# Performance work log

Measured on AMD Instinct MI355X. Metric: run time of the kernel, lower is better.

The kernel has to match this reference:

```python
import jax, jax.numpy as jnp
import numpy as np

B, H, S, D = 2, 16, 2048, 64
SCALE = 1.0 / (D ** 0.5)
MASK_FILL = -1e9


def setup_inputs() -> dict:
    key = jax.random.key(0)
    kq, kk, kv = jax.random.split(key, 3)
    q = jax.random.normal(kq, (B, H, S, D), dtype=jnp.float32)
    k = jax.random.normal(kk, (B, H, S, D), dtype=jnp.float32)
    v = jax.random.normal(kv, (B, H, S, D), dtype=jnp.float32)
    # causal mask: True where attention is disallowed (j > i)
    attn_mask = jnp.triu(jnp.ones((S, S), dtype=jnp.bool_), k=1)[None, None]
    return {"q": q, "k": k, "v": v, "attn_mask": attn_mask}


def reference(q, k, v, attn_mask):
    # scores: [B,H,S,S] = (q @ k^T) * scale, then masked_fill(mask, -1e9)
    scores = jnp.einsum("bhqd,bhkd->bhqk", q, k) * SCALE
    scores = jnp.where(attn_mask, MASK_FILL, scores)
    attn_prob = jax.nn.softmax(scores, axis=-1)  # dropout p=0.0 (eval)
    context = jnp.einsum("bhqk,bhkd->bhqd", attn_prob, v)
    return (context, attn_prob)
```

## Files before the change

### kernel.cpp

```cpp
#include <hip/hip_runtime.h>

#define NB 2
#define NH 16
#define SS 2048
#define DD 64
constexpr float kScale = 0.125f;

typedef __attribute__((ext_vector_type(8))) short bf16x8;
typedef __attribute__((ext_vector_type(4))) float f32x4;

union FragAB { bf16x8 v; unsigned u[4]; };

__device__ __forceinline__ unsigned pack2bf(float lo, float hi) {
  unsigned ul = __float_as_uint(lo) + 0x8000u;
  unsigned uh = __float_as_uint(hi) + 0x8000u;
  return __builtin_amdgcn_perm(uh, ul, 0x07060302u);
}
__device__ __forceinline__ short f2bf(float f) {
  return (short)((__float_as_uint(f) + 0x8000u) >> 16);
}

__global__ __launch_bounds__(256, 3) void attn_mfma(
    const float* __restrict__ Q, const float* __restrict__ K,
    const float* __restrict__ V, float* __restrict__ ctx,
    float* __restrict__ prob) {
  const int qt   = 31 - (blockIdx.x & 31);
  const int bh   = blockIdx.x >> 5;
  const int t    = threadIdx.x;
  const int lane = t & 63;
  const int wave = t >> 6;
  const int quad = lane >> 4;
  const int l16  = lane & 15;

  const int q_base = qt * 64;
  const int i_max  = q_base + 63;
  const int qw     = q_base + wave * 16;
  const size_t hoff = (size_t)bh * SS * DD;
  const float* Kh = K + hoff;
  const float* Vh = V + hoff;

  __shared__ __align__(16) short Vt[2][DD][40];
  __shared__ __align__(16) short Pld[4][16][40];

  FragAB aq[2];
  {
    const float* qp = Q + hoff + (size_t)(qw + l16) * DD + quad * 8;
#pragma unroll
    for (int c = 0; c < 2; ++c) {
      float4 x = *(const float4*)(qp + c * 32);
      float4 y = *(const float4*)(qp + c * 32 + 4);
      aq[c].u[0] = pack2bf(x.x * kScale, x.y * kScale);
      aq[c].u[1] = pack2bf(x.z * kScale, x.w * kScale);
      aq[c].u[2] = pack2bf(y.x * kScale, y.y * kScale);
      aq[c].u[3] = pack2bf(y.z * kScale, y.w * kScale);
    }
  }

  const int irow0 = qw + quad * 4;

  auto qk_e = [&](int j0, f32x4 et[2]) {
#pragma unroll
    for (int tl = 0; tl < 2; ++tl) {
      const float* kp = Kh + (size_t)(j0 + tl * 16 + l16) * DD + quad * 8;
      float4 a = *(const float4*)(kp);
      float4 b = *(const float4*)(kp + 4);
      float4 c2 = *(const float4*)(kp + 32);
      float4 d2 = *(const float4*)(kp + 36);
      FragAB b0, b1;
      b0.u[0] = pack2bf(a.x, a.y);  b0.u[1] = pack2bf(a.z, a.w);
      b0.u[2] = pack2bf(b.x, b.y);  b0.u[3] = pack2bf(b.z, b.w);
      b1.u[0] = pack2bf(c2.x, c2.y); b1.u[1] = pack2bf(c2.z, c2.w);
      b1.u[2] = pack2bf(d2.x, d2.y); b1.u[3] = pack2bf(d2.z, d2.w);
      f32x4 s = {0.f, 0.f, 0.f, 0.f};
      s = __builtin_amdgcn_mfma_f32_16x16x32_bf16(aq[0].v, b0.v, s, 0, 0, 0);
      s = __builtin_amdgcn_mfma_f32_16x16x32_bf16(aq[1].v, b1.v, s, 0, 0, 0);
      const int jc = j0 + tl * 16 + l16;
#pragma unroll
      for (int r = 0; r < 4; ++r)
        et[tl][r] = (jc <= irow0 + r) ? __expf(s[r]) : 0.f;
    }
  };

  const int nc = (i_max + 32) >> 5;

  float l_acc[4] = {0.f, 0.f, 0.f, 0.f};
  for (int c = 0; c < nc; ++c) {
    f32x4 et[2];
    qk_e(c * 32, et);
#pragma unroll
    for (int r = 0; r < 4; ++r) l_acc[r] += et[0][r] + et[1][r];
  }
  float inv_l[4];
#pragma unroll
  for (int r = 0; r < 4; ++r) {
    float s = l_acc[r];
    s += __shfl_xor(s, 1, 64);
    s += __shfl_xor(s, 2, 64);
    s += __shfl_xor(s, 4, 64);
    s += __shfl_xor(s, 8, 64);
    inv_l[r] = 1.f / s;
  }

  const int jj = t >> 3;
  const int d0 = (t & 7) * 8;
  const int cw = jj ^ ((t & 3) << 3);

  f32x4 O[4] = {{0,0,0,0},{0,0,0,0},{0,0,0,0},{0,0,0,0}};

  float4 pv0, pv1;
  {
    const float* vp = Vh + (size_t)jj * DD + d0;
    pv0 = *(const float4*)vp; pv1 = *(const float4*)(vp + 4);
    float tmp[8] = {pv0.x,pv0.y,pv0.z,pv0.w,pv1.x,pv1.y,pv1.z,pv1.w};
#pragma unroll
    for (int i2 = 0; i2 < 8; ++i2) Vt[0][d0 + i2][cw] = f2bf(tmp[i2]);
  }

  for (int c = 0; c < nc; ++c) {
    __syncthreads();
    const int cn = c + 1;
    if (cn < nc) {
      const float* vp = Vh + (size_t)(cn * 32 + jj) * DD + d0;
      pv0 = *(const float4*)vp; pv1 = *(const float4*)(vp + 4);
    }
    const int j0 = c * 32;
    f32x4 et[2];
    qk_e(j0, et);

    float* pb = prob + ((size_t)(bh * SS + irow0) * SS) + j0 + l16;
#pragma unroll
    for (int tl = 0; tl < 2; ++tl) {
#pragma unroll
      for (int r = 0; r < 4; ++r) {
        pb[(size_t)r * SS + tl * 16] = et[tl][r] * inv_l[r];
        Pld[wave][quad * 4 + r][tl * 16 + l16] = f2bf(et[tl][r]);
      }
    }
    FragAB ap;
    ap.v = *(const bf16x8*)&Pld[wave][l16][quad * 8];
    const int vb = c & 1;
#pragma unroll
    for (int n = 0; n < 4; ++n) {
      const int dim = n * 16 + l16;
      const int cb = (quad << 3) ^ (((dim >> 3) & 3) << 3);
      FragAB bv;
      bv.v = *(const bf16x8*)&Vt[vb][dim][cb];
      O[n] = __builtin_amdgcn_mfma_f32_16x16x32_bf16(ap.v, bv.v, O[n], 0, 0, 0);
    }
    if (cn < nc) {
      float tmp[8] = {pv0.x,pv0.y,pv0.z,pv0.w,pv1.x,pv1.y,pv1.z,pv1.w};
#pragma unroll
      for (int i2 = 0; i2 < 8; ++i2) Vt[cn & 1][d0 + i2][cw] = f2bf(tmp[i2]);
    }
  }

  for (int c = nc; c < SS / 32; ++c) {
    float* pb = prob + ((size_t)(bh * SS + irow0) * SS) + c * 32 + l16;
#pragma unroll
    for (int tl = 0; tl < 2; ++tl)
#pragma unroll
      for (int r = 0; r < 4; ++r) pb[(size_t)r * SS + tl * 16] = 0.f;
  }

#pragma unroll
  for (int n = 0; n < 4; ++n)
#pragma unroll
    for (int r = 0; r < 4; ++r)
      ctx[(size_t)(bh * SS + irow0 + r) * DD + n * 16 + l16] = O[n][r] * inv_l[r];
}

extern "C" void kernel_launch(void* const* d_in, const int* in_sizes, int n_in,
                              void* d_out, int out_size, void* d_ws, size_t ws_size,
                              hipStream_t stream) {
  const float* q = (const float*)d_in[0];
  const float* k = (const float*)d_in[1];
  const float* v = (const float*)d_in[2];
  float* ctx  = (float*)d_out;
  float* prob = (float*)d_out + (size_t)NB * NH * SS * DD;

  attn_mfma<<<dim3(NB * NH * 32), dim3(256), 0, stream>>>(q, k, v, ctx, prob);
}
```

Baseline: 978.5 us.

## Single-pass attention with bf16 prob staging in output, K prefetch, XCD-aware block mapping

Drops the separate row-sum pass over K by accumulating the softmax denominator during the single PV pass. Unnormalized probabilities are staged as bf16 in the output's own row buffer and then rescaled and expanded to fp32 in place, which saves recomputing QK^T. It also double-buffers K loads in registers, remaps block indices so each XCD keeps a group of heads and balances the causal tile work, and raises the occupancy hint. The in-place staging relies on careful ordering: it reads packed data at offset c*16 and writes at c*32, iterating backward within each wave's own rows.

```diff
diff --git a/kernel.cpp b/kernel.cpp
--- a/kernel.cpp
+++ b/kernel.cpp
@@ -20,12 +20,22 @@
   return (short)((__float_as_uint(f) + 0x8000u) >> 16);
 }
 
-__global__ __launch_bounds__(256, 3) void attn_mfma(
+struct KC { float4 x[8]; };
+
+__global__ __launch_bounds__(256, 4) void attn_mfma(
     const float* __restrict__ Q, const float* __restrict__ K,
     const float* __restrict__ V, float* __restrict__ ctx,
     float* __restrict__ prob) {
-  const int qt   = 31 - (blockIdx.x & 31);
-  const int bh   = blockIdx.x >> 5;
+  const int b    = blockIdx.x;
+  const int xcd  = b & 7;
+  const int slot = b >> 3;
+  const int oct  = slot >> 5;
+  const int cu5  = slot & 31;
+  const int ww   = cu5 & 7;
+  const int hl   = cu5 >> 3;
+  const int qt   = (3 - oct) * 8 + ((oct & 1) ? (7 - ww) : ww);
+  const int bh   = xcd * 4 + hl;
+
   const int t    = threadIdx.x;
   const int lane = t & 63;
   const int wave = t >> 6;
@@ -41,6 +51,7 @@
 
   __shared__ __align__(16) short Vt[2][DD][40];
   __shared__ __align__(16) short Pld[4][16][40];
+  __shared__ float linv_s[4][20];
 
   FragAB aq[2];
   {
@@ -57,92 +68,88 @@
   }
 
   const int irow0 = qw + quad * 4;
-
-  auto qk_e = [&](int j0, f32x4 et[2]) {
+  const int nc = (i_max + 32) >> 5;
+
+  auto kload = [&](KC& kk, int j0) {
+    const float* kp = Kh + (size_t)(j0 + l16) * DD + quad * 8;
+    kk.x[0] = *(const float4*)(kp);
+    kk.x[1] = *(const float4*)(kp + 4);
+    kk.x[2] = *(const float4*)(kp + 32);
+    kk.x[3] = *(const float4*)(kp + 36);
+    kk.x[4] = *(const float4*)(kp + 16 * DD);
+    kk.x[5] = *(const float4*)(kp + 16 * DD + 4);
+    kk.x[6] = *(const float4*)(kp + 16 * DD + 32);
+    kk.x[7] = *(const float4*)(kp + 16 * DD + 36);
+  };
+
+  auto qke = [&](const KC& kk, int j0, f32x4 et[2]) {
 #pragma unroll
     for (int tl = 0; tl < 2; ++tl) {
-      const float* kp = Kh + (size_t)(j0 + tl * 16 + l16) * DD + quad * 8;
-      float4 a = *(const float4*)(kp);
-      float4 b = *(const float4*)(kp + 4);
-      float4 c2 = *(const float4*)(kp + 32);
-      float4 d2 = *(const float4*)(kp + 36);
+      const float4 a  = kk.x[tl * 4 + 0];
+      const float4 b2 = kk.x[tl * 4 + 1];
+      const float4 cc = kk.x[tl * 4 + 2];
+      const float4 d2 = kk.x[tl * 4 + 3];
       FragAB b0, b1;
-      b0.u[0] = pack2bf(a.x, a.y);  b0.u[1] = pack2bf(a.z, a.w);
-      b0.u[2] = pack2bf(b.x, b.y);  b0.u[3] = pack2bf(b.z, b.w);
-      b1.u[0] = pack2bf(c2.x, c2.y); b1.u[1] = pack2bf(c2.z, c2.w);
+      b0.u[0] = pack2bf(a.x, a.y);   b0.u[1] = pack2bf(a.z, a.w);
+      b0.u[2] = pack2bf(b2.x, b2.y); b0.u[3] = pack2bf(b2.z, b2.w);
+      b1.u[0] = pack2bf(cc.x, cc.y); b1.u[1] = pack2bf(cc.z, cc.w);
       b1.u[2] = pack2bf(d2.x, d2.y); b1.u[3] = pack2bf(d2.z, d2.w);
-      f32x4 s = {0.f, 0.f, 0.f, 0.f};
-      s = __builtin_amdgcn_mfma_f32_16x16x32_bf16(aq[0].v, b0.v, s, 0, 0, 0);
-      s = __builtin_amdgcn_mfma_f32_16x16x32_bf16(aq[1].v, b1.v, s, 0, 0, 0);
+      f32x4 acc = {0.f, 0.f, 0.f, 0.f};
+      acc = __builtin_amdgcn_mfma_f32_16x16x32_bf16(aq[0].v, b0.v, acc, 0, 0, 0);
+      acc = __builtin_amdgcn_mfma_f32_16x16x32_bf16(aq[1].v, b1.v, acc, 0, 0, 0);
       const int jc = j0 + tl * 16 + l16;
 #pragma unroll
       for (int r = 0; r < 4; ++r)
-        et[tl][r] = (jc <= irow0 + r) ? __expf(s[r]) : 0.f;
+        et[tl][r] = (jc <= irow0 + r) ? __expf(acc[r]) : 0.f;
     }
   };
-
-  const int nc = (i_max + 32) >> 5;
-
-  float l_acc[4] = {0.f, 0.f, 0.f, 0.f};
-  for (int c = 0; c < nc; ++c) {
-    f32x4 et[2];
-    qk_e(c * 32, et);
-#pragma unroll
-    for (int r = 0; r < 4; ++r) l_acc[r] += et[0][r] + et[1][r];
-  }
-  float inv_l[4];
-#pragma unroll
-  for (int r = 0; r < 4; ++r) {
-    float s = l_acc[r];
-    s += __shfl_xor(s, 1, 64);
-    s += __shfl_xor(s, 2, 64);
-    s += __shfl_xor(s, 4, 64);
-    s += __shfl_xor(s, 8, 64);
-    inv_l[r] = 1.f / s;
-  }
 
   const int jj = t >> 3;
   const int d0 = (t & 7) * 8;
   const int cw = jj ^ ((t & 3) << 3);
 
   f32x4 O[4] = {{0,0,0,0},{0,0,0,0},{0,0,0,0},{0,0,0,0}};
-
-  float4 pv0, pv1;
+  float l_acc[4] = {0.f, 0.f, 0.f, 0.f};
+  float* ppk = prob + (size_t)(bh * SS + qw + l16) * SS;
+
   {
     const float* vp = Vh + (size_t)jj * DD + d0;
-    pv0 = *(const float4*)vp; pv1 = *(const float4*)(vp + 4);
+    float4 pv0 = *(const float4*)vp, pv1 = *(const float4*)(vp + 4);
     float tmp[8] = {pv0.x,pv0.y,pv0.z,pv0.w,pv1.x,pv1.y,pv1.z,pv1.w};
 #pragma unroll
     for (int i2 = 0; i2 < 8; ++i2) Vt[0][d0 + i2][cw] = f2bf(tmp[i2]);
   }
 
-  for (int c = 0; c < nc; ++c) {
+  KC ka, kb;
+  kload(ka, 0);
+
+  auto body = [&](int c, const KC& kc, KC& kn, bool pf) {
     __syncthreads();
     const int cn = c + 1;
+    float4 pv0, pv1;
     if (cn < nc) {
       const float* vp = Vh + (size_t)(cn * 32 + jj) * DD + d0;
       pv0 = *(const float4*)vp; pv1 = *(const float4*)(vp + 4);
     }
-    const int j0 = c * 32;
+    if (pf) kload(kn, cn * 32);
     f32x4 et[2];
-    qk_e(j0, et);
-
-    float* pb = prob + ((size_t)(bh * SS + irow0) * SS) + j0 + l16;
-#pragma unroll
-    for (int tl = 0; tl < 2; ++tl) {
-#pragma unroll
-      for (int r = 0; r < 4; ++r) {
-        pb[(size_t)r * SS + tl * 16] = et[tl][r] * inv_l[r];
+    qke(kc, c * 32, et);
+#pragma unroll
+    for (int r = 0; r < 4; ++r) l_acc[r] += et[0][r] + et[1][r];
+#pragma unroll
+    for (int tl = 0; tl < 2; ++tl)
+#pragma unroll
+      for (int r = 0; r < 4; ++r)
         Pld[wave][quad * 4 + r][tl * 16 + l16] = f2bf(et[tl][r]);
-      }
-    }
     FragAB ap;
     ap.v = *(const bf16x8*)&Pld[wave][l16][quad * 8];
+    uint4 pk; pk.x = ap.u[0]; pk.y = ap.u[1]; pk.z = ap.u[2]; pk.w = ap.u[3];
+    *reinterpret_cast<uint4*>(ppk + c * 16 + quad * 4) = pk;
     const int vb = c & 1;
 #pragma unroll
     for (int n = 0; n < 4; ++n) {
       const int dim = n * 16 + l16;
-      const int cb = (quad << 3) ^ (((dim >> 3) & 3) << 3);
+      const int cb = (quad << 3) ^ ((((dim >> 3) & 3)) << 3);
       FragAB bv;
       bv.v = *(const bf16x8*)&Vt[vb][dim][cb];
       O[n] = __builtin_amdgcn_mfma_f32_16x16x32_bf16(ap.v, bv.v, O[n], 0, 0, 0);
@@ -152,21 +159,62 @@
 #pragma unroll
       for (int i2 = 0; i2 < 8; ++i2) Vt[cn & 1][d0 + i2][cw] = f2bf(tmp[i2]);
     }
-  }
-
-  for (int c = nc; c < SS / 32; ++c) {
-    float* pb = prob + ((size_t)(bh * SS + irow0) * SS) + c * 32 + l16;
-#pragma unroll
-    for (int tl = 0; tl < 2; ++tl)
-#pragma unroll
-      for (int r = 0; r < 4; ++r) pb[(size_t)r * SS + tl * 16] = 0.f;
-  }
+  };
+
+  {
+    int c = 0;
+    for (; c + 2 <= nc; c += 2) {
+      body(c, ka, kb, true);
+      body(c + 1, kb, ka, c + 2 < nc);
+    }
+    if (c < nc) body(c, ka, kb, false);
+  }
+
+  float inv_l[4];
+#pragma unroll
+  for (int r = 0; r < 4; ++r) {
+    float s2 = l_acc[r];
+    s2 += __shfl_xor(s2, 1, 64);
+    s2 += __shfl_xor(s2, 2, 64);
+    s2 += __shfl_xor(s2, 4, 64);
+    s2 += __shfl_xor(s2, 8, 64);
+    inv_l[r] = 1.f / s2;
+  }
+  if (l16 < 4) linv_s[wave][quad * 4 + l16] = inv_l[l16];
 
 #pragma unroll
   for (int n = 0; n < 4; ++n)
 #pragma unroll
     for (int r = 0; r < 4; ++r)
       ctx[(size_t)(bh * SS + irow0 + r) * DD + n * 16 + l16] = O[n][r] * inv_l[r];
+
+  asm volatile("" ::: "memory");
+  __builtin_amdgcn_s_waitcnt(0);
+  asm volatile("" ::: "memory");
+
+  const int prow = lane & 15;
+  const int cg   = lane >> 4;
+  const float lv = linv_s[wave][prow];
+  float* pr = prob + (size_t)(bh * SS + qw + prow) * SS;
+  for (int c = nc - 1; c >= 0; --c) {
+    const uint4 pk = *reinterpret_cast<const uint4*>(pr + c * 16 + cg * 4);
+    float4 o0, o1;
+    o0.x = __uint_as_float(pk.x << 16) * lv;
+    o0.y = __uint_as_float(pk.x & 0xffff0000u) * lv;
+    o0.z = __uint_as_float(pk.y << 16) * lv;
+    o0.w = __uint_as_float(pk.y & 0xffff0000u) * lv;
+    o1.x = __uint_as_float(pk.z << 16) * lv;
+    o1.y = __uint_as_float(pk.z & 0xffff0000u) * lv;
+    o1.z = __uint_as_float(pk.w << 16) * lv;
+    o1.w = __uint_as_float(pk.w & 0xffff0000u) * lv;
+    *reinterpret_cast<float4*>(pr + c * 32 + cg * 8) = o0;
+    *reinterpret_cast<float4*>(pr + c * 32 + cg * 8 + 4) = o1;
+  }
+  const float4 z4 = {0.f, 0.f, 0.f, 0.f};
+  for (int c = nc; c < SS / 32; ++c) {
+    *reinterpret_cast<float4*>(pr + c * 32 + cg * 8) = z4;
+    *reinterpret_cast<float4*>(pr + c * 32 + cg * 8 + 4) = z4;
+  }
 }
 
 extern "C" void kernel_launch(void* const* d_in, const int* in_sizes, int n_in,
@@ -177,6 +225,5 @@
   const float* v = (const float*)d_in[2];
   float* ctx  = (float*)d_out;
   float* prob = (float*)d_out + (size_t)NB * NH * SS * DD;
-
   attn_mfma<<<dim3(NB * NH * 32), dim3(256), 0, stream>>>(q, k, v, ctx, prob);
 }
```

Result: faster. 878.9 us (-10.2%).
